# Kernel tuning notes

Measured on AMD Instinct MI355X. Metric: run time of the kernel, lower is better.

The kernel has to match this reference:

```python
import jax, jax.numpy as jnp
import numpy as np

GRID = 0.5
N_GRID = (48, 48, 48)
K = 14  # max bbox extent: floor(2 + 2*1.5*1.7/0.5) + 1 = 13, +1 slack
E2 = float(np.exp(2.0))


def _splat(vecs, r):
    """Scatter-add per-atom vdW kernels into a (48,48,48) grid. vecs: [N,3]."""
    ngf = jnp.asarray(N_GRID, jnp.float32)
    ngi = jnp.asarray(N_GRID, jnp.int32)
    vec = vecs + ngf * 0.5 - 0.5                      # [N,3] shifted coords
    b = 1.5 * r
    # int() in torch truncates toward zero; astype(int32) matches, and the
    # clip to [0, n_grid] makes the negative-value difference irrelevant.
    min_pt = jnp.clip(((vec - b) / GRID).astype(jnp.int32), 0, ngi)   # [N,3]
    max_pt = jnp.clip((2.0 + (vec + b) / GRID).astype(jnp.int32), 0, ngi)
    offs = jnp.arange(K, dtype=jnp.int32)
    idx = min_pt[:, None, :] + offs[None, :, None]    # [N,K,3]
    valid = idx < max_pt[:, None, :]                  # [N,K,3] (idx >= min_pt >= 0)
    dax = vec[:, None, :] - GRID * idx.astype(jnp.float32)  # [N,K,3]
    d2ax = dax * dax
    # dense per-atom distance blocks [N,K,K,K]
    d2 = (d2ax[:, :, None, None, 0]
          + d2ax[:, None, :, None, 1]
          + d2ax[:, None, None, :, 2])
    d = jnp.sqrt(d2)
    r2 = r * r
    f1 = jnp.exp(-2.0 * d2 / r2)
    f2 = 4.0 * d2 / (E2 * r2) - 12.0 * d / (E2 * r) + 9.0 / E2
    val = jnp.where(d < r, f1, jnp.where(d < 1.5 * r, f2, 0.0))
    m = (valid[:, :, None, None, 0]
         & valid[:, None, :, None, 1]
         & valid[:, None, None, :, 2])
    val = jnp.where(m, val, 0.0)
    ic = jnp.minimum(idx, ngi - 1)                    # keep indices in-bounds (masked anyway)
    out = jnp.zeros(N_GRID, jnp.float32)
    return out.at[ic[:, :, None, None, 0],
                  ic[:, None, :, None, 1],
                  ic[:, None, None, :, 2]].add(val)


def setup_inputs() -> dict:
    key = jax.random.key(0)
    kC, kN, kO = jax.random.split(key, 3)
    N = 16384
    # atoms uniform inside the 24A box centered at origin
    mk = lambda k: jax.random.uniform(k, (N, 3), jnp.float32, -12.0, 12.0)
    return {"vecs_C": mk(kC), "vecs_N": mk(kN), "vecs_O": mk(kO)}


def reference(vecs_C, vecs_N, vecs_O):
    return jnp.stack([_splat(vecs_C, 1.7),
                      _splat(vecs_N, 1.55),
                      _splat(vecs_O, 1.52)], axis=0)  # [3,48,48,48]
```

## Files before the change

kernel.cpp:

```cpp
#include <hip/hip_runtime.h>

#define NG 48
#define NT 6
#define NTILES (NT * NT * NT)
#define CHUNK 512
#define NCHUNK 32
#define SUBCAP 96
#define NSEG 8
#define CPSEG (NCHUNK / NSEG)
#define LISTS_OFF  131072
#define COPIES_OFF (8u << 20)

__device__ __forceinline__ float type_r(int type) {
    return (type == 0) ? 1.7f : ((type == 1) ? 1.55f : 1.52f);
}

__global__ __launch_bounds__(512) void bin_kernel(
    const float* __restrict__ vC, const float* __restrict__ vN,
    const float* __restrict__ vO, int* __restrict__ cntc,
    unsigned short* __restrict__ lists, int natoms)
{
    const int type  = blockIdx.y;
    const int chunk = blockIdx.x;
    const float r = type_r(type);
    const float b = 1.5f * r + 1e-3f;
    const float* __restrict__ vecs = (type == 0) ? vC : ((type == 1) ? vN : vO);
    const int tid  = threadIdx.x;
    const int atom = chunk * CHUNK + tid;

    __shared__ int lfill[NTILES];
    if (tid < NTILES) lfill[tid] = 0;
    __syncthreads();

    int x0 = 1, x1 = 0, y0 = 1, y1 = 0, z0 = 1, z1 = 0;
    if (atom < natoms) {
        const float vx = vecs[3 * atom + 0] + 23.5f;
        const float vy = vecs[3 * atom + 1] + 23.5f;
        const float vz = vecs[3 * atom + 2] + 23.5f;
        x0 = max(0,      (int)floorf((vx - 3.5f - b) * 0.25f) + 1);
        x1 = min(NT - 1, (int)ceilf ((vx + b)        * 0.25f) - 1);
        y0 = max(0,      (int)floorf((vy - 3.5f - b) * 0.25f) + 1);
        y1 = min(NT - 1, (int)ceilf ((vy + b)        * 0.25f) - 1);
        z0 = max(0,      (int)floorf((vz - 3.5f - b) * 0.25f) + 1);
        z1 = min(NT - 1, (int)ceilf ((vz + b)        * 0.25f) - 1);
    }
    const bool has = (x0 <= x1) & (y0 <= y1) & (z0 <= z1);

    if (has)
        for (int tx = x0; tx <= x1; ++tx)
            for (int ty = y0; ty <= y1; ++ty)
                for (int tz = z0; tz <= z1; ++tz) {
                    const int tl = (tx * NT + ty) * NT + tz;
                    const int p  = atomicAdd(&lfill[tl], 1);
                    if (p < SUBCAP)
                        lists[((size_t)(type * NTILES + tl) * NCHUNK + chunk)
                              * SUBCAP + p] = (unsigned short)atom;
                }
    __syncthreads();

    if (tid < NTILES)
        cntc[(type * NTILES + tid) * NCHUNK + chunk] = min(lfill[tid], SUBCAP);
}

__global__ __launch_bounds__(256) void gather_seg(
    const float* __restrict__ vC, const float* __restrict__ vN,
    const float* __restrict__ vO, const int* __restrict__ cntc,
    const unsigned short* __restrict__ lists, float* __restrict__ copies)
{
    const int type = blockIdx.y;
    const int s = blockIdx.x / NTILES;
    const int t = blockIdx.x - s * NTILES;
    const int lt = type * NTILES + t;

    __shared__ int ps[CPSEG + 1];
    __shared__ float4 sa[256];

    const int tid = threadIdx.x;
    if (tid == 0) {
        int acc = 0;
        ps[0] = 0;
        #pragma unroll
        for (int c = 0; c < CPSEG; ++c) {
            acc += cntc[lt * NCHUNK + s * CPSEG + c];
            ps[c + 1] = acc;
        }
    }
    __syncthreads();
    const int total = ps[CPSEG];
    if (total == 0) return;

    const float r = type_r(type);
    const float* __restrict__ vecs = (type == 0) ? vC : ((type == 1) ? vN : vO);

    const int tx = t / (NT * NT);
    const int ty = (t / NT) % NT;
    const int tz = t % NT;
    const int lx  = tid >> 6;
    const int ly  = (tid >> 3) & 7;
    const int lz  = tid & 7;

    const float b      = 1.5f * r;
    const float r15sq  = b * b;
    const float rr     = r * r;
    const float E2     = 7.3890562f;
    const float c2a    = 4.0f / (E2 * rr);
    const float c2b    = 12.0f / (E2 * r);
    const float c2c    = 9.0f / E2;
    const float n2orr  = -2.0f / rr;

    const float px0 = 0.5f * (float)(tx * 8 + lx);
    const float px1 = px0 + 2.0f;
    const float py  = 0.5f * (float)(ty * 8 + ly);
    const float pz  = 0.5f * (float)(tz * 8 + lz);

    const unsigned short* __restrict__ lbase =
        lists + ((size_t)lt * NCHUNK + s * CPSEG) * SUBCAP;

    float acc0 = 0.0f, acc1 = 0.0f;

    for (int base = 0; base < total; base += 256) {
        const int m = min(256, total - base);
        if (tid < m) {
            const int g = base + tid;
            int c = (ps[2] <= g) ? 2 : 0;
            c += (ps[c + 1] <= g) ? 1 : 0;
            const int idx = (int)lbase[(size_t)c * SUBCAP + (g - ps[c])];
            sa[tid] = make_float4(vecs[3 * idx + 0] + 23.5f,
                                  vecs[3 * idx + 1] + 23.5f,
                                  vecs[3 * idx + 2] + 23.5f, 0.0f);
        }
        __syncthreads();

        for (int j = 0; j < m; ++j) {
            const float4 a = sa[j];
            const float dy  = a.y - py;
            const float dz  = a.z - pz;
            const float syz = fmaf(dy, dy, dz * dz);
            const float dx0 = a.x - px0;
            const float d2a = fmaf(dx0, dx0, syz);
            const float dx1 = a.x - px1;
            const float d2b = fmaf(dx1, dx1, syz);
            const bool h0 = d2a < r15sq;
            const bool h1 = d2b < r15sq;
            if (__ballot(h0 | h1) == 0ull) continue;
            if (h0) {
                const float d = sqrtf(d2a);
                acc0 += (d < r) ? __expf(n2orr * d2a)
                                : fmaf(c2a, d2a, fmaf(-c2b, d, c2c));
            }
            if (h1) {
                const float d = sqrtf(d2b);
                acc1 += (d < r) ? __expf(n2orr * d2b)
                                : fmaf(c2a, d2b, fmaf(-c2b, d, c2c));
            }
        }
        __syncthreads();
    }

    float* __restrict__ cp = copies + ((size_t)lt * NSEG + s) * 512;
    cp[tid]       = acc0;
    cp[tid + 256] = acc1;
}

__global__ __launch_bounds__(256) void reduce_kernel(
    const int* __restrict__ cntc, const float* __restrict__ copies,
    float* __restrict__ out)
{
    const int type = blockIdx.y;
    const int t = blockIdx.x;
    const int lt = type * NTILES + t;
    const int tid = threadIdx.x;

    __shared__ int segact[NSEG];
    if (tid < NSEG) {
        int acc = 0;
        #pragma unroll
        for (int c = 0; c < CPSEG; ++c)
            acc += cntc[lt * NCHUNK + tid * CPSEG + c];
        segact[tid] = acc;
    }
    __syncthreads();

    const float* __restrict__ cp = copies + ((size_t)lt * NSEG) * 512;
    float o0 = 0.0f, o1 = 0.0f;
    #pragma unroll
    for (int ss = 0; ss < NSEG; ++ss) {
        if (segact[ss] > 0) {
            o0 += cp[(size_t)ss * 512 + tid];
            o1 += cp[(size_t)ss * 512 + 256 + tid];
        }
    }

    const int tx = t / (NT * NT);
    const int ty = (t / NT) % NT;
    const int tz = t % NT;
    const int lx  = tid >> 6;
    const int ly  = (tid >> 3) & 7;
    const int lz  = tid & 7;
    const int X0 = tx * 8 + lx;
    const int Y  = ty * 8 + ly;
    const int Z  = tz * 8 + lz;
    float* __restrict__ o = out + (size_t)type * NG * NG * NG;
    o[((X0      * NG) + Y) * NG + Z] = o0;
    o[(((X0 + 4) * NG) + Y) * NG + Z] = o1;
}

extern "C" void kernel_launch(void* const* d_in, const int* in_sizes, int n_in,
                              void* d_out, int out_size, void* d_ws, size_t ws_size,
                              hipStream_t stream) {
    const float* vC = (const float*)d_in[0];
    const float* vN = (const float*)d_in[1];
    const float* vO = (const float*)d_in[2];
    float* out = (float*)d_out;

    int* cntc = (int*)d_ws;
    unsigned short* lists = (unsigned short*)((char*)d_ws + LISTS_OFF);
    float* copies = (float*)((char*)d_ws + COPIES_OFF);

    const int natoms = in_sizes[0] / 3;
    const int nchunk = (natoms + CHUNK - 1) / CHUNK;

    dim3 bgrid(nchunk, 3, 1);
    bin_kernel<<<bgrid, CHUNK, 0, stream>>>(vC, vN, vO, cntc, lists, natoms);

    dim3 ggrid(NTILES * NSEG, 3, 1);
    gather_seg<<<ggrid, 256, 0, stream>>>(vC, vN, vO, cntc, lists, copies);

    dim3 rgrid(NTILES, 3, 1);
    reduce_kernel<<<rgrid, 256, 0, stream>>>(cntc, copies, out);
}
```

Before: 39.50 us.

## Give each gather thread a 2x2 voxel micro-tile with 128-thread blocks

Shrinks the gather block from 256 to 128 threads, with each thread now accumulating four voxels (two x planes and two z planes) instead of two. This reuses the per-atom dy/dz/dx partial squares across more voxels and halves the number of atoms staged per batch. The per-segment prefix sum moves from a single thread in shared memory to a vectorized int4 load held in registers, which removes one barrier, and the trailing loop barrier is folded into the next iteration. The cost is fewer threads per block, more registers per thread, and a coarser ballot skip that covers four voxels at once.

```diff
diff --git a/kernel.cpp b/kernel.cpp
--- a/kernel.cpp
+++ b/kernel.cpp
@@ -62,7 +62,7 @@
         cntc[(type * NTILES + tid) * NCHUNK + chunk] = min(lfill[tid], SUBCAP);
 }
 
-__global__ __launch_bounds__(256) void gather_seg(
+__global__ __launch_bounds__(128) void gather_seg(
     const float* __restrict__ vC, const float* __restrict__ vN,
     const float* __restrict__ vO, const int* __restrict__ cntc,
     const unsigned short* __restrict__ lists, float* __restrict__ copies)
@@ -71,22 +71,14 @@
     const int s = blockIdx.x / NTILES;
     const int t = blockIdx.x - s * NTILES;
     const int lt = type * NTILES + t;
-
-    __shared__ int ps[CPSEG + 1];
-    __shared__ float4 sa[256];
-
     const int tid = threadIdx.x;
-    if (tid == 0) {
-        int acc = 0;
-        ps[0] = 0;
-        #pragma unroll
-        for (int c = 0; c < CPSEG; ++c) {
-            acc += cntc[lt * NCHUNK + s * CPSEG + c];
-            ps[c + 1] = acc;
-        }
-    }
-    __syncthreads();
-    const int total = ps[CPSEG];
+
+    const int4 c4 = *reinterpret_cast<const int4*>(
+        &cntc[lt * NCHUNK + s * CPSEG]);
+    const int e0 = c4.x;
+    const int e1 = e0 + c4.y;
+    const int e2 = e1 + c4.z;
+    const int total = e2 + c4.w;
     if (total == 0) return;
 
     const float r = type_r(type);
@@ -95,9 +87,9 @@
     const int tx = t / (NT * NT);
     const int ty = (t / NT) % NT;
     const int tz = t % NT;
-    const int lx  = tid >> 6;
-    const int ly  = (tid >> 3) & 7;
-    const int lz  = tid & 7;
+    const int lx = tid >> 5;
+    const int ly = (tid >> 2) & 7;
+    const int lz = tid & 3;
 
     const float b      = 1.5f * r;
     const float r15sq  = b * b;
@@ -109,22 +101,24 @@
     const float n2orr  = -2.0f / rr;
 
     const float px0 = 0.5f * (float)(tx * 8 + lx);
-    const float px1 = px0 + 2.0f;
     const float py  = 0.5f * (float)(ty * 8 + ly);
-    const float pz  = 0.5f * (float)(tz * 8 + lz);
-
+    const float pz0 = 0.5f * (float)(tz * 8 + lz);
+
+    __shared__ float4 sa[128];
     const unsigned short* __restrict__ lbase =
         lists + ((size_t)lt * NCHUNK + s * CPSEG) * SUBCAP;
 
-    float acc0 = 0.0f, acc1 = 0.0f;
-
-    for (int base = 0; base < total; base += 256) {
-        const int m = min(256, total - base);
+    float acc00 = 0.0f, acc01 = 0.0f, acc10 = 0.0f, acc11 = 0.0f;
+
+    for (int base = 0; base < total; base += 128) {
+        const int m = min(128, total - base);
+        if (base) __syncthreads();
         if (tid < m) {
             const int g = base + tid;
-            int c = (ps[2] <= g) ? 2 : 0;
-            c += (ps[c + 1] <= g) ? 1 : 0;
-            const int idx = (int)lbase[(size_t)c * SUBCAP + (g - ps[c])];
+            int c; int off;
+            if (g < e1) { c = (g < e0) ? 0 : 1; off = (g < e0) ? 0 : e0; }
+            else        { c = (g < e2) ? 2 : 3; off = (g < e2) ? e1 : e2; }
+            const int idx = (int)lbase[(size_t)c * SUBCAP + (g - off)];
             sa[tid] = make_float4(vecs[3 * idx + 0] + 23.5f,
                                   vecs[3 * idx + 1] + 23.5f,
                                   vecs[3 * idx + 2] + 23.5f, 0.0f);
@@ -134,32 +128,36 @@
         for (int j = 0; j < m; ++j) {
             const float4 a = sa[j];
             const float dy  = a.y - py;
-            const float dz  = a.z - pz;
-            const float syz = fmaf(dy, dy, dz * dz);
-            const float dx0 = a.x - px0;
-            const float d2a = fmaf(dx0, dx0, syz);
-            const float dx1 = a.x - px1;
-            const float d2b = fmaf(dx1, dx1, syz);
-            const bool h0 = d2a < r15sq;
-            const bool h1 = d2b < r15sq;
-            if (__ballot(h0 | h1) == 0ull) continue;
-            if (h0) {
-                const float d = sqrtf(d2a);
-                acc0 += (d < r) ? __expf(n2orr * d2a)
-                                : fmaf(c2a, d2a, fmaf(-c2b, d, c2c));
-            }
-            if (h1) {
-                const float d = sqrtf(d2b);
-                acc1 += (d < r) ? __expf(n2orr * d2b)
-                                : fmaf(c2a, d2b, fmaf(-c2b, d, c2c));
-            }
+            const float sy  = dy * dy;
+            const float dz0 = a.z - pz0, dz1 = dz0 - 2.0f;
+            const float sz0 = fmaf(dz0, dz0, sy), sz1 = fmaf(dz1, dz1, sy);
+            const float dx0 = a.x - px0, dx1 = dx0 - 2.0f;
+            const float xx0 = dx0 * dx0, xx1 = dx1 * dx1;
+            const float d200 = xx0 + sz0, d201 = xx0 + sz1;
+            const float d210 = xx1 + sz0, d211 = xx1 + sz1;
+            const bool h00 = d200 < r15sq, h01 = d201 < r15sq;
+            const bool h10 = d210 < r15sq, h11 = d211 < r15sq;
+            if (__ballot(h00 | h01 | h10 | h11) == 0ull) continue;
+            if (h00) { const float d = sqrtf(d200);
+                acc00 += (d < r) ? __expf(n2orr * d200)
+                                 : fmaf(c2a, d200, fmaf(-c2b, d, c2c)); }
+            if (h01) { const float d = sqrtf(d201);
+                acc01 += (d < r) ? __expf(n2orr * d201)
+                                 : fmaf(c2a, d201, fmaf(-c2b, d, c2c)); }
+            if (h10) { const float d = sqrtf(d210);
+                acc10 += (d < r) ? __expf(n2orr * d210)
+                                 : fmaf(c2a, d210, fmaf(-c2b, d, c2c)); }
+            if (h11) { const float d = sqrtf(d211);
+                acc11 += (d < r) ? __expf(n2orr * d211)
+                                 : fmaf(c2a, d211, fmaf(-c2b, d, c2c)); }
         }
-        __syncthreads();
     }
 
     float* __restrict__ cp = copies + ((size_t)lt * NSEG + s) * 512;
-    cp[tid]       = acc0;
-    cp[tid + 256] = acc1;
+    cp[((lx      * 8) + ly) * 8 + lz]      = acc00;
+    cp[((lx      * 8) + ly) * 8 + lz + 4]  = acc01;
+    cp[(((lx + 4) * 8) + ly) * 8 + lz]     = acc10;
+    cp[(((lx + 4) * 8) + ly) * 8 + lz + 4] = acc11;
 }
 
 __global__ __launch_bounds__(256) void reduce_kernel(
@@ -194,9 +192,9 @@
     const int tx = t / (NT * NT);
     const int ty = (t / NT) % NT;
     const int tz = t % NT;
-    const int lx  = tid >> 6;
-    const int ly  = (tid >> 3) & 7;
-    const int lz  = tid & 7;
+    const int lx = tid >> 6;
+    const int ly = (tid >> 3) & 7;
+    const int lz = tid & 7;
     const int X0 = tx * 8 + lx;
     const int Y  = ty * 8 + ly;
     const int Z  = tz * 8 + lz;
@@ -224,7 +222,7 @@
     bin_kernel<<<bgrid, CHUNK, 0, stream>>>(vC, vN, vO, cntc, lists, natoms);
 
     dim3 ggrid(NTILES * NSEG, 3, 1);
-    gather_seg<<<ggrid, 256, 0, stream>>>(vC, vN, vO, cntc, lists, copies);
+    gather_seg<<<ggrid, 128, 0, stream>>>(vC, vN, vO, cntc, lists, copies);
 
     dim3 rgrid(NTILES, 3, 1);
     reduce_kernel<<<rgrid, 256, 0, stream>>>(cntc, copies, out);
```

Measured after the change: 46.60 us. +18.0%, slower.
